# Optimization experiments

Hardware: AMD Instinct MI355X
Metric: run time of the kernel (lower is better)

Reference implementation:

```python
import jax, jax.numpy as jnp
import numpy as np

B, H, W, C = 8, 64, 64, 256
RC = C // 8  # reduced channels per build()

def setup_inputs() -> dict:
    key = jax.random.key(0)
    ks = jax.random.split(key, 4)
    x = jax.random.normal(ks[0], (B, H, W, C), dtype=jnp.float32)
    # 1x1 conv kernels flattened to [Cin, Cout]; glorot-ish scale
    wq = jax.random.normal(ks[1], (C, RC), dtype=jnp.float32) * (1.0 / np.sqrt(C))
    wk = jax.random.normal(ks[2], (C, RC), dtype=jnp.float32) * (1.0 / np.sqrt(C))
    wv = jax.random.normal(ks[3], (C, C), dtype=jnp.float32) * (1.0 / np.sqrt(C))
    bq = jnp.zeros((RC,), dtype=jnp.float32)
    bk = jnp.zeros((RC,), dtype=jnp.float32)
    bv = jnp.zeros((C,), dtype=jnp.float32)
    return {"x": x, "wq": wq, "bq": bq, "wk": wk, "bk": bk, "wv": wv, "bv": bv}

def reference(x, wq, bq, wk, bk, wv, bv):
    b, h, w, c = x.shape
    n = h * w
    # 1x1 convs == per-pixel channel matmuls; q/k have relu activation, v does not
    q = jax.nn.relu(jnp.einsum('bhwc,cd->bhwd', x, wq) + bq).reshape(b, n, -1)  # [B,N,RC]
    k = jax.nn.relu(jnp.einsum('bhwc,cd->bhwd', x, wk) + bk).reshape(b, n, -1)  # [B,N,RC]
    v = (jnp.einsum('bhwc,cd->bhwd', x, wv) + bv).reshape(b, n, c)              # [B,N,C]
    attn = jax.nn.softmax(jnp.einsum('bnd,bmd->bnm', q, k), axis=-1)            # [B,N,N]
    out = jnp.einsum('bnm,bmc->bnc', attn, v).reshape(b, h, w, c)
    return out + x
```

## Files before the change

### kernel.cpp

```cpp
#include <hip/hip_runtime.h>
#include <hip/hip_bf16.h>

typedef __attribute__((ext_vector_type(8))) short s16x8;
typedef __attribute__((ext_vector_type(4))) float f32x4;
typedef __attribute__((ext_vector_type(4))) unsigned int u32x4;

#define BATCH 8
#define NPIX  4096
#define CCH   256
#define RCH   32
#define TK    32
#define HALFK 2048
#define NIT   (HALFK / TK)
#define THR   8.0f
#define LOG2E 1.4426950408889634f
#define XPAD  264

__device__ __forceinline__ unsigned short f2bf(float f) {
  __hip_bfloat16 h = __float2bfloat16(f);
  return __builtin_bit_cast(unsigned short, h);
}

__device__ __forceinline__ unsigned int cvt_pk(float lo, float hi) {
  unsigned int r;
  asm("v_cvt_pk_bf16_f32 %0, %1, %2" : "=v"(r) : "v"(lo), "v"(hi));
  return r;
}

__device__ __forceinline__ void gload_lds16(const void* g, void* l) {
  __builtin_amdgcn_global_load_lds(
      (const __attribute__((address_space(1))) void*)g,
      (__attribute__((address_space(3))) void*)l, 16, 0, 0);
}

__global__ void wprep_kernel(const float* __restrict__ wq,
                             const float* __restrict__ wk,
                             const float* __restrict__ wv,
                             unsigned short* __restrict__ wqkT,
                             unsigned short* __restrict__ wvT) {
  int stride = gridDim.x * blockDim.x;
  int i0 = blockIdx.x * blockDim.x + threadIdx.x;
  for (int i = i0; i < 64 * CCH; i += stride) {
    int d = i >> 8, c = i & 255;
    float v = (d < RCH) ? wq[c * RCH + d] : wk[c * RCH + (d - RCH)];
    wqkT[i] = f2bf(v);
  }
  for (int i = i0; i < CCH * CCH; i += stride) {
    int d = i >> 8, c = i & 255;
    wvT[i] = f2bf(wv[c * CCH + d]);
  }
}

__global__ __launch_bounds__(256)
void proj_kernel(const float* __restrict__ x,
                 const unsigned short* __restrict__ wqkT,
                 const unsigned short* __restrict__ wvT,
                 const float* __restrict__ bq,
                 const float* __restrict__ bk,
                 const float* __restrict__ bv,
                 unsigned short* __restrict__ qb,
                 unsigned short* __restrict__ kb,
                 unsigned short* __restrict__ vT) {
  __shared__ __attribute__((aligned(16))) unsigned short Xt[64 * XPAD];

  int t = threadIdx.x;
  int w = t >> 6, l = t & 63, g = l >> 4, lc = l & 15;
  f32x4 zero = {0.f, 0.f, 0.f, 0.f};

  if (blockIdx.x < 512) {
    int row0 = blockIdx.x * 64;
    #pragma unroll
    for (int i = 0; i < 16; ++i) {
      int flat4 = i * 256 + t;
      int row = flat4 >> 6, col4 = flat4 & 63;
      float4 v = *reinterpret_cast<const float4*>(
          x + ((size_t)(row0 + row)) * CCH + col4 * 4);
      ushort4 o4;
      o4.x = f2bf(v.x); o4.y = f2bf(v.y); o4.z = f2bf(v.z); o4.w = f2bf(v.w);
      *reinterpret_cast<ushort4*>(&Xt[row * XPAD + col4 * 4]) = o4;
    }
    __syncthreads();

    f32x4 acc[4];
    for (int ct = 0; ct < 4; ++ct) acc[ct] = zero;
    for (int ks = 0; ks < 8; ++ks) {
      s16x8 a = *reinterpret_cast<const s16x8*>(
          &Xt[(w * 16 + lc) * XPAD + ks * 32 + g * 8]);
      for (int ct = 0; ct < 4; ++ct) {
        s16x8 bfr = *reinterpret_cast<const s16x8*>(
            wqkT + (size_t)(ct * 16 + lc) * CCH + ks * 32 + g * 8);
        acc[ct] = __builtin_amdgcn_mfma_f32_16x16x32_bf16(a, bfr, acc[ct], 0, 0, 0);
      }
    }
    for (int ct = 0; ct < 4; ++ct) {
      int col = ct * 16 + lc;
      float bias = (col < RCH) ? bq[col] : bk[col - RCH];
      for (int r = 0; r < 4; ++r) {
        int row = row0 + w * 16 + 4 * g + r;
        float v = fmaxf(acc[ct][r] + bias, 0.f);
        if (col < RCH) qb[(size_t)row * RCH + col] = f2bf(v * LOG2E);
        else           kb[(size_t)row * RCH + (col - RCH)] = f2bf(v);
      }
    }
  } else {
    int idx = blockIdx.x - 512;
    int b = idx & 7; idx >>= 3;
    int dt = idx & 3; int nt = idx >> 2;
    int d0 = dt * 64 + w * 16;
    int n0 = nt * 64;
    #pragma unroll
    for (int i = 0; i < 16; ++i) {
      int flat4 = i * 256 + t;
      int row = flat4 >> 6, col4 = flat4 & 63;
      float4 v = *reinterpret_cast<const float4*>(
          x + ((size_t)b * NPIX + n0 + row) * CCH + col4 * 4);
      ushort4 o4;
      o4.x = f2bf(v.x); o4.y = f2bf(v.y); o4.z = f2bf(v.z); o4.w = f2bf(v.w);
      *reinterpret_cast<ushort4*>(&Xt[row * XPAD + col4 * 4]) = o4;
    }
    __syncthreads();

    f32x4 acc[4];
    for (int ct = 0; ct < 4; ++ct) acc[ct] = zero;
    for (int ks = 0; ks < 8; ++ks) {
      s16x8 a = *reinterpret_cast<const s16x8*>(
          wvT + (size_t)(d0 + lc) * CCH + ks * 32 + g * 8);
      for (int ct = 0; ct < 4; ++ct) {
        s16x8 bfr = *reinterpret_cast<const s16x8*>(
            &Xt[(ct * 16 + lc) * XPAD + ks * 32 + g * 8]);
        acc[ct] = __builtin_amdgcn_mfma_f32_16x16x32_bf16(a, bfr, acc[ct], 0, 0, 0);
      }
    }
    for (int ct = 0; ct < 4; ++ct) {
      for (int r = 0; r < 4; ++r) {
        int d = d0 + 4 * g + r;
        int n = n0 + ct * 16 + lc;
        vT[((size_t)b * CCH + d) * NPIX + n] = f2bf(acc[ct][r] + bv[d]);
      }
    }
  }
}

__global__ __launch_bounds__(256, 2)
void attn_kernel(const unsigned short* __restrict__ qb,
                 const unsigned short* __restrict__ kb,
                 const unsigned short* __restrict__ vT,
                 const float* __restrict__ x,
                 float* __restrict__ out) {
  __shared__ __attribute__((aligned(16))) unsigned short Vlds[2][CCH * 64];
  __shared__ __attribute__((aligned(16))) float mergeLS[2][32];
  __shared__ float mLds[2];

  int b  = blockIdx.x & 7;
  int qt = blockIdx.x >> 3;
  int t  = threadIdx.x;
  int w = t >> 6, l = t & 63, g = l >> 4, lc = l & 15;
  int a = w >> 1, s = w & 1;
  const size_t bN = (size_t)b * NPIX;
  f32x4 zero = {0.f, 0.f, 0.f, 0.f};

  const unsigned short* kbase = kb + bN * RCH;
  const unsigned short* vbase = vT + (size_t)b * CCH * NPIX;

  int qbase = qt * 64 + a * 32;
  s16x8 qfA = *reinterpret_cast<const s16x8*>(qb + (bN + qbase + lc) * RCH + g * 8);
  s16x8 qfB = *reinterpret_cast<const s16x8*>(qb + (bN + qbase + 16 + lc) * RCH + g * 8);

  int chb = t >> 3, gr = t & 7;
  int gsw = gr ^ (chb & 7);
  int koff = (gsw < 4) ? (gsw * 8) : (HALFK + (gsw - 4) * 8);
  const unsigned short* vsrc = vbase + (size_t)chb * NPIX + koff;

  int krb = 8 * (lc >> 2) + (lc & 3);
  int kO  = s * HALFK + krb;

  unsigned int swz = (lc & 7) << 4;
  int vrS = (s * 64 + g * 16) ^ swz;

  s16x8 ones;
  #pragma unroll
  for (int i = 0; i < 8; ++i) ones[i] = (short)0x3F80;

  f32x4 o[2][16];
  #pragma unroll
  for (int qh = 0; qh < 2; ++qh)
    #pragma unroll
    for (int cc = 0; cc < 16; ++cc) o[qh][cc] = zero;
  f32x4 ols[2];
  ols[0] = zero; ols[1] = zero;
  float m = -1e30f;

  #pragma unroll
  for (int i = 0; i < 8; ++i)
    gload_lds16(vsrc + (size_t)i * 32 * NPIX,
                (char*)&Vlds[0][0] + i * 4096 + t * 16);
  s16x8 kf0 = *reinterpret_cast<const s16x8*>(kbase + (size_t)(kO + 0) * RCH + g * 8);
  s16x8 kf1 = *reinterpret_cast<const s16x8*>(kbase + (size_t)(kO + 4) * RCH + g * 8);
  __syncthreads();

  for (int it = 0; it < NIT; ++it) {
    int p = it & 1;
    int kv = it * TK;
    bool nx = (it + 1) < NIT;

    if (nx) {
      #pragma unroll
      for (int i = 0; i < 8; ++i)
        gload_lds16(vsrc + kv + TK + (size_t)i * 32 * NPIX,
                    (char*)&Vlds[p ^ 1][0] + i * 4096 + t * 16);
    }

    f32x4 sA0 = __builtin_amdgcn_mfma_f32_16x16x32_bf16(kf0, qfA, zero, 0, 0, 0);
    f32x4 sA1 = __builtin_amdgcn_mfma_f32_16x16x32_bf16(kf1, qfA, zero, 0, 0, 0);
    f32x4 sB0 = __builtin_amdgcn_mfma_f32_16x16x32_bf16(kf0, qfB, zero, 0, 0, 0);
    f32x4 sB1 = __builtin_amdgcn_mfma_f32_16x16x32_bf16(kf1, qfB, zero, 0, 0, 0);

    if (nx) {
      kf0 = *reinterpret_cast<const s16x8*>(
          kbase + (size_t)(kO + kv + TK + 0) * RCH + g * 8);
      kf1 = *reinterpret_cast<const s16x8*>(
          kbase + (size_t)(kO + kv + TK + 4) * RCH + g * 8);
    }

    float xA = fmaxf(fmaxf(sA0[0], sA0[1]), fmaxf(sA0[2], sA0[3]));
    float xB = fmaxf(fmaxf(sA1[0], sA1[1]), fmaxf(sA1[2], sA1[3]));
    float xC = fmaxf(fmaxf(sB0[0], sB0[1]), fmaxf(sB0[2], sB0[3]));
    float xD = fmaxf(fmaxf(sB1[0], sB1[1]), fmaxf(sB1[2], sB1[3]));
    float pmax = fmaxf(fmaxf(xA, xB), fmaxf(xC, xD));

    float sc = 1.f;
    int resc = !__all(pmax - m <= THR);
    if (resc) {
      #pragma unroll
      for (int off = 1; off <= 32; off <<= 1)
        pmax = fmaxf(pmax, __shfl_xor(pmax, off));
      float mnew = fmaxf(m, pmax);
      sc = exp2f(m - mnew);
      m = mnew;
    }

    unsigned int pkA[4], pkB[4];
    pkA[0] = cvt_pk(exp2f(sA0[0] - m), exp2f(sA0[1] - m));
    pkA[1] = cvt_pk(exp2f(sA0[2] - m), exp2f(sA0[3] - m));
    pkA[2] = cvt_pk(exp2f(sA1[0] - m), exp2f(sA1[1] - m));
    pkA[3] = cvt_pk(exp2f(sA1[2] - m), exp2f(sA1[3] - m));
    pkB[0] = cvt_pk(exp2f(sB0[0] - m), exp2f(sB0[1] - m));
    pkB[1] = cvt_pk(exp2f(sB0[2] - m), exp2f(sB0[3] - m));
    pkB[2] = cvt_pk(exp2f(sB1[0] - m), exp2f(sB1[1] - m));
    pkB[3] = cvt_pk(exp2f(sB1[2] - m), exp2f(sB1[3] - m));

    if (resc) {
      #pragma unroll
      for (int qh = 0; qh < 2; ++qh) {
        #pragma unroll
        for (int cc = 0; cc < 16; ++cc)
          #pragma unroll
          for (int r = 0; r < 4; ++r) o[qh][cc][r] *= sc;
        #pragma unroll
        for (int r = 0; r < 4; ++r) ols[qh][r] *= sc;
      }
    }

    u32x4 uA = {pkA[0], pkA[1], pkA[2], pkA[3]};
    u32x4 uB = {pkB[0], pkB[1], pkB[2], pkB[3]};
    s16x8 paA = __builtin_bit_cast(s16x8, uA);
    s16x8 paB = __builtin_bit_cast(s16x8, uB);
    const char* pb = (const char*)&Vlds[p][0] + lc * 128 + vrS;
    __builtin_amdgcn_s_setprio(1);
    ols[0] = __builtin_amdgcn_mfma_f32_16x16x32_bf16(paA, ones, ols[0], 0, 0, 0);
    ols[1] = __builtin_amdgcn_mfma_f32_16x16x32_bf16(paB, ones, ols[1], 0, 0, 0);
    #pragma unroll
    for (int cc = 0; cc < 16; ++cc) {
      s16x8 vb = *reinterpret_cast<const s16x8*>(pb + cc * 2048);
      o[0][cc] = __builtin_amdgcn_mfma_f32_16x16x32_bf16(paA, vb, o[0][cc], 0, 0, 0);
      o[1][cc] = __builtin_amdgcn_mfma_f32_16x16x32_bf16(paB, vb, o[1][cc], 0, 0, 0);
    }
    __builtin_amdgcn_s_setprio(0);

    __syncthreads();
  }

  if (s == 1) {
    if (lc == 0) {
      *reinterpret_cast<f32x4*>(&mergeLS[a][4 * g])      = ols[0];
      *reinterpret_cast<f32x4*>(&mergeLS[a][16 + 4 * g]) = ols[1];
    }
    if (l == 0) mLds[a] = m;
  }
  __syncthreads();

  float* mrg = (float*)&Vlds[0][0];
  if (s == 1) {
    float* base = mrg + a * 8192 + l * 128;
    #pragma unroll
    for (int qh = 0; qh < 2; ++qh)
      #pragma unroll
      for (int cc = 0; cc < 16; ++cc) {
        int idx = qh * 16 + cc;
        *reinterpret_cast<f32x4*>(base + ((idx + l) & 31) * 4) = o[qh][cc];
      }
  }
  __syncthreads();
  if (s == 0) {
    float mB = mLds[a];
    float mT = fmaxf(m, mB);
    float sAc = exp2f(m - mT), sBc = exp2f(mB - mT);
    const float* base = mrg + a * 8192 + l * 128;
    #pragma unroll
    for (int qh = 0; qh < 2; ++qh) {
      f32x4 lB4 = *reinterpret_cast<const f32x4*>(&mergeLS[a][qh * 16 + 4 * g]);
      f32x4 rl;
      #pragma unroll
      for (int r = 0; r < 4; ++r)
        rl[r] = 1.0f / (ols[qh][r] * sAc + lB4[r] * sBc);
      #pragma unroll
      for (int cc = 0; cc < 16; ++cc) {
        int idx = qh * 16 + cc;
        f32x4 ob = *reinterpret_cast<const f32x4*>(base + ((idx + l) & 31) * 4);
        #pragma unroll
        for (int r = 0; r < 4; ++r) {
          size_t row = bN + qbase + qh * 16 + 4 * g + r;
          size_t oi = row * CCH + cc * 16 + lc;
          out[oi] = (o[qh][cc][r] * sAc + ob[r] * sBc) * rl[r] + x[oi];
        }
      }
    }
  }
}

extern "C" void kernel_launch(void* const* d_in, const int* in_sizes, int n_in,
                              void* d_out, int out_size, void* d_ws, size_t ws_size,
                              hipStream_t stream) {
  const float* x  = (const float*)d_in[0];
  const float* wq = (const float*)d_in[1];
  const float* bq = (const float*)d_in[2];
  const float* wk = (const float*)d_in[3];
  const float* bk = (const float*)d_in[4];
  const float* wv = (const float*)d_in[5];
  const float* bv = (const float*)d_in[6];
  float* out = (float*)d_out;

  unsigned short* ws   = (unsigned short*)d_ws;
  unsigned short* qb   = ws;
  unsigned short* kb   = qb + 1048576;
  unsigned short* vT   = kb + 1048576;
  unsigned short* wqkT = vT + 8388608;
  unsigned short* wvT  = wqkT + 16384;

  wprep_kernel<<<dim3(80), dim3(256), 0, stream>>>(wq, wk, wv, wqkT, wvT);
  proj_kernel<<<dim3(2560), dim3(256), 0, stream>>>(x, wqkT, wvT, bq, bk, bv,
                                                    qb, kb, vT);
  attn_kernel<<<dim3(512), dim3(256), 0, stream>>>(qb, kb, vT, x, out);
}
```

Measured before the change: 139.8 us.

## Halve query tile per block, single-buffer V in LDS, raise occupancy to four blocks

```diff
diff --git a/kernel.cpp b/kernel.cpp
--- a/kernel.cpp
+++ b/kernel.cpp
@@ -141,14 +141,14 @@
   }
 }
 
-__global__ __launch_bounds__(256, 2)
+__global__ __launch_bounds__(256, 4)
 void attn_kernel(const unsigned short* __restrict__ qb,
                  const unsigned short* __restrict__ kb,
                  const unsigned short* __restrict__ vT,
                  const float* __restrict__ x,
                  float* __restrict__ out) {
-  __shared__ __attribute__((aligned(16))) unsigned short Vlds[2][CCH * 64];
-  __shared__ __attribute__((aligned(16))) float mergeLS[2][32];
+  __shared__ __attribute__((aligned(16))) unsigned short Vlds[CCH * 64];
+  __shared__ __attribute__((aligned(16))) float mergeLS[2][16];
   __shared__ float mLds[2];
 
   int b  = blockIdx.x & 7;
@@ -162,9 +162,8 @@
   const unsigned short* kbase = kb + bN * RCH;
   const unsigned short* vbase = vT + (size_t)b * CCH * NPIX;
 
-  int qbase = qt * 64 + a * 32;
-  s16x8 qfA = *reinterpret_cast<const s16x8*>(qb + (bN + qbase + lc) * RCH + g * 8);
-  s16x8 qfB = *reinterpret_cast<const s16x8*>(qb + (bN + qbase + 16 + lc) * RCH + g * 8);
+  int qbase = qt * 32 + a * 16;
+  s16x8 qf = *reinterpret_cast<const s16x8*>(qb + (bN + qbase + lc) * RCH + g * 8);
 
   int chb = t >> 3, gr = t & 7;
   int gsw = gr ^ (chb & 7);
@@ -181,52 +180,42 @@
   #pragma unroll
   for (int i = 0; i < 8; ++i) ones[i] = (short)0x3F80;
 
-  f32x4 o[2][16];
+  f32x4 o[16];
   #pragma unroll
-  for (int qh = 0; qh < 2; ++qh)
-    #pragma unroll
-    for (int cc = 0; cc < 16; ++cc) o[qh][cc] = zero;
-  f32x4 ols[2];
-  ols[0] = zero; ols[1] = zero;
+  for (int cc = 0; cc < 16; ++cc) o[cc] = zero;
+  f32x4 ols = zero;
   float m = -1e30f;
 
-  #pragma unroll
-  for (int i = 0; i < 8; ++i)
-    gload_lds16(vsrc + (size_t)i * 32 * NPIX,
-                (char*)&Vlds[0][0] + i * 4096 + t * 16);
   s16x8 kf0 = *reinterpret_cast<const s16x8*>(kbase + (size_t)(kO + 0) * RCH + g * 8);
   s16x8 kf1 = *reinterpret_cast<const s16x8*>(kbase + (size_t)(kO + 4) * RCH + g * 8);
-  __syncthreads();
 
   for (int it = 0; it < NIT; ++it) {
-    int p = it & 1;
     int kv = it * TK;
-    bool nx = (it + 1) < NIT;
-
-    if (nx) {
-      #pragma unroll
-      for (int i = 0; i < 8; ++i)
-        gload_lds16(vsrc + kv + TK + (size_t)i * 32 * NPIX,
-                    (char*)&Vlds[p ^ 1][0] + i * 4096 + t * 16);
-    }
-
-    f32x4 sA0 = __builtin_amdgcn_mfma_f32_16x16x32_bf16(kf0, qfA, zero, 0, 0, 0);
-    f32x4 sA1 = __builtin_amdgcn_mfma_f32_16x16x32_bf16(kf1, qfA, zero, 0, 0, 0);
-    f32x4 sB0 = __builtin_amdgcn_mfma_f32_16x16x32_bf16(kf0, qfB, zero, 0, 0, 0);
-    f32x4 sB1 = __builtin_amdgcn_mfma_f32_16x16x32_bf16(kf1, qfB, zero, 0, 0, 0);
-
-    if (nx) {
+
+    asm volatile("s_waitcnt lgkmcnt(0)" ::: "memory");
+    __builtin_amdgcn_s_barrier();
+    asm volatile("" ::: "memory");
+
+    #pragma unroll
+    for (int i = 0; i < 8; ++i)
+      gload_lds16(vsrc + kv + (size_t)i * 32 * NPIX,
+                  (char*)&Vlds[0] + i * 4096 + t * 16);
+    __builtin_amdgcn_sched_barrier(0);
+
+    f32x4 s0 = __builtin_amdgcn_mfma_f32_16x16x32_bf16(kf0, qf, zero, 0, 0, 0);
+    f32x4 s1 = __builtin_amdgcn_mfma_f32_16x16x32_bf16(kf1, qf, zero, 0, 0, 0);
+
+    {
+      int kv2 = (kv + TK) & (HALFK - 1);
       kf0 = *reinterpret_cast<const s16x8*>(
-          kbase + (size_t)(kO + kv + TK + 0) * RCH + g * 8);
+          kbase + (size_t)(kO + kv2 + 0) * RCH + g * 8);
       kf1 = *reinterpret_cast<const s16x8*>(
-          kbase + (size_t)(kO + kv + TK + 4) * RCH + g * 8);
-    }
-
-    float xA = fmaxf(fmaxf(sA0[0], sA0[1]), fmaxf(sA0[2], sA0[3]));
-    float xB = fmaxf(fmaxf(sA1[0], sA1[1]), fmaxf(sA1[2], sA1[3]));
-    float xC = fmaxf(fmaxf(sB0[0], sB0[1]), fmaxf(sB0[2], sB0[3]));
-    float xD = fmaxf(fmaxf(sB1[0], sB1[1]), fmaxf(sB1[2], sB1[3]));
-    float pmax = fmaxf(fmaxf(xA, xB), fmaxf(xC, xD));
+          kbase + (size_t)(kO + kv2 + 4) * RCH + g * 8);
+    }
+
+    float xA = fmaxf(fmaxf(s0[0], s0[1]), fmaxf(s0[2], s0[3]));
+    float xB = fmaxf(fmaxf(s1[0], s1[1]), fmaxf(s1[2], s1[3]));
+    float pmax = fmaxf(xA, xB);
 
     float sc = 1.f;
     int resc = !__all(pmax - m <= THR);
@@ -239,90 +228,71 @@
       m = mnew;
     }
 
-    unsigned int pkA[4], pkB[4];
-    pkA[0] = cvt_pk(exp2f(sA0[0] - m), exp2f(sA0[1] - m));
-    pkA[1] = cvt_pk(exp2f(sA0[2] - m), exp2f(sA0[3] - m));
-    pkA[2] = cvt_pk(exp2f(sA1[0] - m), exp2f(sA1[1] - m));
-    pkA[3] = cvt_pk(exp2f(sA1[2] - m), exp2f(sA1[3] - m));
-    pkB[0] = cvt_pk(exp2f(sB0[0] - m), exp2f(sB0[1] - m));
-    pkB[1] = cvt_pk(exp2f(sB0[2] - m), exp2f(sB0[3] - m));
-    pkB[2] = cvt_pk(exp2f(sB1[0] - m), exp2f(sB1[1] - m));
-    pkB[3] = cvt_pk(exp2f(sB1[2] - m), exp2f(sB1[3] - m));
+    unsigned int pk0 = cvt_pk(exp2f(s0[0] - m), exp2f(s0[1] - m));
+    unsigned int pk1 = cvt_pk(exp2f(s0[2] - m), exp2f(s0[3] - m));
+    unsigned int pk2 = cvt_pk(exp2f(s1[0] - m), exp2f(s1[1] - m));
+    unsigned int pk3 = cvt_pk(exp2f(s1[2] - m), exp2f(s1[3] - m));
+    u32x4 ua = {pk0, pk1, pk2, pk3};
+    s16x8 pa = __builtin_bit_cast(s16x8, ua);
 
     if (resc) {
       #pragma unroll
-      for (int qh = 0; qh < 2; ++qh) {
+      for (int cc = 0; cc < 16; ++cc)
         #pragma unroll
-        for (int cc = 0; cc < 16; ++cc)
-          #pragma unroll
-          for (int r = 0; r < 4; ++r) o[qh][cc][r] *= sc;
-        #pragma unroll
-        for (int r = 0; r < 4; ++r) ols[qh][r] *= sc;
-      }
-    }
-
-    u32x4 uA = {pkA[0], pkA[1], pkA[2], pkA[3]};
-    u32x4 uB = {pkB[0], pkB[1], pkB[2], pkB[3]};
-    s16x8 paA = __builtin_bit_cast(s16x8, uA);
-    s16x8 paB = __builtin_bit_cast(s16x8, uB);
-    const char* pb = (const char*)&Vlds[p][0] + lc * 128 + vrS;
+        for (int r = 0; r < 4; ++r) o[cc][r] *= sc;
+      #pragma unroll
+      for (int r = 0; r < 4; ++r) ols[r] *= sc;
+    }
+
+    ols = __builtin_amdgcn_mfma_f32_16x16x32_bf16(pa, ones, ols, 0, 0, 0);
+
+    asm volatile("s_waitcnt vmcnt(2)" ::: "memory");
+    __builtin_amdgcn_s_barrier();
+    asm volatile("" ::: "memory");
+
+    const char* pb = (const char*)&Vlds[0] + lc * 128 + vrS;
     __builtin_amdgcn_s_setprio(1);
-    ols[0] = __builtin_amdgcn_mfma_f32_16x16x32_bf16(paA, ones, ols[0], 0, 0, 0);
-    ols[1] = __builtin_amdgcn_mfma_f32_16x16x32_bf16(paB, ones, ols[1], 0, 0, 0);
     #pragma unroll
     for (int cc = 0; cc < 16; ++cc) {
       s16x8 vb = *reinterpret_cast<const s16x8*>(pb + cc * 2048);
-      o[0][cc] = __builtin_amdgcn_mfma_f32_16x16x32_bf16(paA, vb, o[0][cc], 0, 0, 0);
-      o[1][cc] = __builtin_amdgcn_mfma_f32_16x16x32_bf16(paB, vb, o[1][cc], 0, 0, 0);
+      o[cc] = __builtin_amdgcn_mfma_f32_16x16x32_bf16(pa, vb, o[cc], 0, 0, 0);
     }
     __builtin_amdgcn_s_setprio(0);
-
-    __syncthreads();
   }
 
   if (s == 1) {
-    if (lc == 0) {
-      *reinterpret_cast<f32x4*>(&mergeLS[a][4 * g])      = ols[0];
-      *reinterpret_cast<f32x4*>(&mergeLS[a][16 + 4 * g]) = ols[1];
-    }
+    if (lc == 0)
+      *reinterpret_cast<f32x4*>(&mergeLS[a][4 * g]) = ols;
     if (l == 0) mLds[a] = m;
   }
   __syncthreads();
 
-  float* mrg = (float*)&Vlds[0][0];
+  float* mrg = (float*)&Vlds[0];
   if (s == 1) {
-    float* base = mrg + a * 8192 + l * 128;
-    #pragma unroll
-    for (int qh = 0; qh < 2; ++qh)
-      #pragma unroll
-      for (int cc = 0; cc < 16; ++cc) {
-        int idx = qh * 16 + cc;
-        *reinterpret_cast<f32x4*>(base + ((idx + l) & 31) * 4) = o[qh][cc];
-      }
+    float* base = mrg + a * 4096 + l * 64;
+    #pragma unroll
+    for (int cc = 0; cc < 16; ++cc)
+      *reinterpret_cast<f32x4*>(base + ((cc + l) & 15) * 4) = o[cc];
   }
   __syncthreads();
   if (s == 0) {
     float mB = mLds[a];
     float mT = fmaxf(m, mB);
     float sAc = exp2f(m - mT), sBc = exp2f(mB - mT);
-    const float* base = mrg + a * 8192 + l * 128;
-    #pragma unroll
-    for (int qh = 0; qh < 2; ++qh) {
-      f32x4 lB4 = *reinterpret_cast<const f32x4*>(&mergeLS[a][qh * 16 + 4 * g]);
-      f32x4 rl;
+    const float* base = mrg + a * 4096 + l * 64;
+    f32x4 lB4 = *reinterpret_cast<const f32x4*>(&mergeLS[a][4 * g]);
+    f32x4 rl;
+    #pragma unroll
+    for (int r = 0; r < 4; ++r)
+      rl[r] = 1.0f / (ols[r] * sAc + lB4[r] * sBc);
+    #pragma unroll
+    for (int cc = 0; cc < 16; ++cc) {
+      f32x4 ob = *reinterpret_cast<const f32x4*>(base + ((cc + l) & 15) * 4);
       #pragma unroll
-      for (int r = 0; r < 4; ++r)
-        rl[r] = 1.0f / (ols[qh][r] * sAc + lB4[r] * sBc);
-      #pragma unroll
-      for (int cc = 0; cc < 16; ++cc) {
-        int idx = qh * 16 + cc;
-        f32x4 ob = *reinterpret_cast<const f32x4*>(base + ((idx + l) & 31) * 4);
-        #pragma unroll
-        for (int r = 0; r < 4; ++r) {
-          size_t row = bN + qbase + qh * 16 + 4 * g + r;
-          size_t oi = row * CCH + cc * 16 + lc;
-          out[oi] = (o[qh][cc][r] * sAc + ob[r] * sBc) * rl[r] + x[oi];
-        }
+      for (int r = 0; r < 4; ++r) {
+        size_t row = bN + qbase + 4 * g + r;
+        size_t oi = row * CCH + cc * 16 + lc;
+        out[oi] = (o[cc][r] * sAc + ob[r] * sBc) * rl[r] + x[oi];
       }
     }
   }
@@ -350,5 +320,5 @@
   wprep_kernel<<<dim3(80), dim3(256), 0, stream>>>(wq, wk, wv, wqkT, wvT);
   proj_kernel<<<dim3(2560), dim3(256), 0, stream>>>(x, wqkT, wvT, bq, bk, bv,
                                                     qb, kb, vT);
-  attn_kernel<<<dim3(512), dim3(256), 0, stream>>>(qb, kb, vT, x, out);
-}
+  attn_kernel<<<dim3(1024), dim3(256), 0, stream>>>(qb, kb, vT, x, out);
+}
```

Measured after the change: 194.5 us. 39.2% more time.
